# Kernel optimization log

Hardware: AMD Instinct MI355X
Metric: run time of the kernel (lower is better)

Reference implementation:

```python
import jax, jax.numpy as jnp
import numpy as np

B, S, E, H = 4, 2048, 1024, 16
D = E // H  # head_dim = 64

def setup_inputs() -> dict:
    key = jax.random.key(0)
    k1, k2, k3 = jax.random.split(key, 3)
    x = jax.random.normal(k1, (B, S, E), dtype=jnp.float32)
    # nn.Linear(E, 3E, bias=False): y = x @ W^T; we store W already transposed as [E, 3E]
    w_qkv = jax.random.normal(k2, (E, 3 * E), dtype=jnp.float32) * (E ** -0.5)
    w_out = jax.random.normal(k3, (E, E), dtype=jnp.float32) * (E ** -0.5)
    b_out = jnp.zeros((E,), dtype=jnp.float32)
    return {"x": x, "w_qkv": w_qkv, "w_out": w_out, "b_out": b_out}

def reference(x, w_qkv, w_out, b_out):
    b, s, e = x.shape
    h, d = H, e // H
    # qkv projection then rearrange 'b s (qkv h d) -> qkv b h s d'
    qkv = (x @ w_qkv).reshape(b, s, 3, h, d).transpose(2, 0, 3, 1, 4)
    q, k, v = qkv[0], qkv[1], qkv[2]            # each [b, h, s, d]
    scale = jnp.asarray(d, x.dtype) ** -0.5
    att = jnp.einsum('bhxd,bhyd->bhxy', q, k) * scale   # [b, h, s, s]
    att = jax.nn.softmax(att, axis=-1)
    o = jnp.einsum('bhxy,bhyd->bhxd', att, v)           # [b, h, s, d]
    o = o.transpose(0, 2, 1, 3).reshape(b, s, e)        # 'b h s d -> b s (h d)'
    return o @ w_out + b_out
```

## Files before the change

kernel.cpp:

```cpp
#include <hip/hip_runtime.h>
#include <cstdint>
#include <cstddef>


typedef __attribute__((ext_vector_type(8))) short short8;
typedef __attribute__((ext_vector_type(4))) float float4_;
typedef unsigned int u32;
typedef unsigned short u16;

__device__ __forceinline__ u16 f2b(float f) {
  u32 u = __float_as_uint(f);
  u += 0x7FFFu + ((u >> 16) & 1u);
  return (u16)(u >> 16);
}

__device__ __forceinline__ float fexp2(float x) {
#if __has_builtin(__builtin_amdgcn_exp2f)
  return __builtin_amdgcn_exp2f(x);
#else
  return exp2f(x);
#endif
}

__device__ __forceinline__ u32 pk_trunc(float lo, float hi) {
#if __has_builtin(__builtin_amdgcn_perm)
  return __builtin_amdgcn_perm(__float_as_uint(hi), __float_as_uint(lo), 0x07060302);
#else
  return (__float_as_uint(hi) & 0xFFFF0000u) | (__float_as_uint(lo) >> 16);
#endif
}

__device__ __forceinline__ void async_cp16(const void* g, void* l) {
  __builtin_amdgcn_global_load_lds(
      (const __attribute__((address_space(1))) u32*)g,
      (__attribute__((address_space(3))) u32*)l, 16, 0, 0);
}


__global__ void cvt_x_bf16(const float* __restrict__ in, u16* __restrict__ out, int n4) {
  int i = blockIdx.x * 256 + threadIdx.x;
  if (i >= n4) return;
  float4 v = ((const float4*)in)[i];
  uint2 p;
  p.x = (u32)f2b(v.x) | ((u32)f2b(v.y) << 16);
  p.y = (u32)f2b(v.z) | ((u32)f2b(v.w) << 16);
  ((uint2*)out)[i] = p;
}

__global__ void transpose_bf16(const float* __restrict__ in, u16* __restrict__ out,
                               int R, int C) {
  __shared__ float t[32][33];
  int tx = threadIdx.x & 31, ty = threadIdx.x >> 5;
  int r0 = blockIdx.y * 32, c0 = blockIdx.x * 32;
#pragma unroll
  for (int k = 0; k < 4; k++)
    t[ty + 8 * k][tx] = in[(size_t)(r0 + ty + 8 * k) * C + c0 + tx];
  __syncthreads();
#pragma unroll
  for (int k = 0; k < 4; k++)
    out[(size_t)(c0 + ty + 8 * k) * R + r0 + tx] = f2b(t[tx][ty + 8 * k]);
}

__global__ void transpose_v(const u16* __restrict__ V, u16* __restrict__ Vt) {
  __shared__ u16 t[64][80];
  int bh = blockIdx.y, s0 = blockIdx.x * 64;
  const u16* Vh = V + (size_t)bh * 2048 * 64;
  u16* Vth = Vt + (size_t)bh * 64 * 2048;
  int tr = threadIdx.x >> 3;
  int tc = (threadIdx.x & 7) * 8;
#pragma unroll
  for (int p = 0; p < 2; p++) {
    int r = p * 32 + tr;
    *(uint4*)&t[r][tc] = *(const uint4*)(Vh + (size_t)(s0 + r) * 64 + tc);
  }
  __syncthreads();
#pragma unroll
  for (int p = 0; p < 2; p++) {
    int d = p * 32 + tr;
    u16 tmp[8];
#pragma unroll
    for (int k = 0; k < 8; k++) tmp[k] = t[tc + k][d];
    *(uint4*)(Vth + (size_t)d * 2048 + s0 + tc) = *(uint4*)tmp;
  }
}


__global__ __launch_bounds__(256) void gemm_qkv_kernel(
    const u16* __restrict__ A, const u16* __restrict__ Bt,
    u16* __restrict__ QKV) {
  const int K = 1024;
  __shared__ short8 lA[2][512];
  __shared__ short8 lB[2][512];
  int tid = threadIdx.x;
  int w = tid >> 6, l = tid & 63, lr = l & 15, lq = l >> 4;
  int gid = blockIdx.x;
  int xcd = gid & 7, j = gid >> 3;
  int yloc = j & 7, xt = j >> 3;
  int m0 = (xcd * 8 + yloc) * 128, n0 = xt * 128;
  int wm = w & 1, wn = w >> 1;
  float4_ acc[4][4] = {};

  const u16* gA0 = A + (size_t)(m0 + w * 32 + lr) * K + lq * 8;
  const u16* gA1 = gA0 + 16 * K;
  const u16* gB0 = Bt + (size_t)(n0 + w * 32 + lr) * K + lq * 8;
  const u16* gB1 = gB0 + 16 * K;

  auto stage = [&](int buf, int k0) {
    async_cp16(gA0 + k0, &lA[buf][(w * 2 + 0) * 64 + l]);
    async_cp16(gA1 + k0, &lA[buf][(w * 2 + 1) * 64 + l]);
    async_cp16(gB0 + k0, &lB[buf][(w * 2 + 0) * 64 + l]);
    async_cp16(gB1 + k0, &lB[buf][(w * 2 + 1) * 64 + l]);
  };
  auto compute = [&](int buf) {
    short8 af[4], bf[4];
#pragma unroll
    for (int t = 0; t < 4; t++) {
      af[t] = lA[buf][(wm * 4 + t) * 64 + l];
      bf[t] = lB[buf][(wn * 4 + t) * 64 + l];
    }
#pragma unroll
    for (int mt = 0; mt < 4; mt++)
#pragma unroll
      for (int nt = 0; nt < 4; nt++)
        acc[mt][nt] = __builtin_amdgcn_mfma_f32_16x16x32_bf16(af[mt], bf[nt], acc[mt][nt], 0, 0, 0);
  };

  stage(0, 0);
  for (int k0 = 0; k0 < K; k0 += 64) {
    __syncthreads();
    stage(1, k0 + 32);
    compute(0);
    __syncthreads();
    if (k0 + 64 < K) stage(0, k0 + 64);
    compute(1);
  }

  const float qsc = 0.18033688011112042f;
#pragma unroll
  for (int nt = 0; nt < 4; nt++) {
    int gn = n0 + wn * 64 + nt * 16 + lr;
    int sel = gn >> 10;
    int h = (gn >> 6) & 15;
    int d = gn & 63;
    float sc = (sel == 0) ? qsc : 1.0f;
    u16* dst = QKV + (size_t)sel * 8388608 + ((size_t)h * 2048) * 64 + d;
#pragma unroll
    for (int mt = 0; mt < 4; mt++) {
#pragma unroll
      for (int r = 0; r < 4; r++) {
        int gm = m0 + wm * 64 + mt * 16 + lq * 4 + r;
        int b = gm >> 11, s = gm & 2047;
        dst[((size_t)b * 16 * 2048 + s) * 64] = f2b(acc[mt][nt][r] * sc);
      }
    }
  }
}

__global__ __launch_bounds__(256) void gemm_out_kernel(
    const u16* __restrict__ A, const u16* __restrict__ Bt,
    const float* __restrict__ bias, float* __restrict__ out) {
  const int K = 1024;
  __shared__ short8 lA[2][512];
  __shared__ short8 lB[2][512];
  int tid = threadIdx.x;
  int w = tid >> 6, l = tid & 63, lr = l & 15, lq = l >> 4;
  int gid = blockIdx.x;
  int xcd = gid & 7, j = gid >> 3;
  int yloc = j & 7, xt = j >> 3;
  int m0 = (xcd * 8 + yloc) * 128, n0 = xt * 128;
  int wm = w & 1, wn = w >> 1;
  float4_ acc[4][4] = {};

  const u16* gA0 = A + (size_t)(m0 + w * 32 + lr) * K + lq * 8;
  const u16* gA1 = gA0 + 16 * K;
  const u16* gB0 = Bt + (size_t)(n0 + w * 32 + lr) * K + lq * 8;
  const u16* gB1 = gB0 + 16 * K;

  auto stage = [&](int buf, int k0) {
    async_cp16(gA0 + k0, &lA[buf][(w * 2 + 0) * 64 + l]);
    async_cp16(gA1 + k0, &lA[buf][(w * 2 + 1) * 64 + l]);
    async_cp16(gB0 + k0, &lB[buf][(w * 2 + 0) * 64 + l]);
    async_cp16(gB1 + k0, &lB[buf][(w * 2 + 1) * 64 + l]);
  };
  auto compute = [&](int buf) {
    short8 af[4], bf[4];
#pragma unroll
    for (int t = 0; t < 4; t++) {
      af[t] = lA[buf][(wm * 4 + t) * 64 + l];
      bf[t] = lB[buf][(wn * 4 + t) * 64 + l];
    }
#pragma unroll
    for (int mt = 0; mt < 4; mt++)
#pragma unroll
      for (int nt = 0; nt < 4; nt++)
        acc[mt][nt] = __builtin_amdgcn_mfma_f32_16x16x32_bf16(af[mt], bf[nt], acc[mt][nt], 0, 0, 0);
  };

  stage(0, 0);
  for (int k0 = 0; k0 < K; k0 += 64) {
    __syncthreads();
    stage(1, k0 + 32);
    compute(0);
    __syncthreads();
    if (k0 + 64 < K) stage(0, k0 + 64);
    compute(1);
  }

#pragma unroll
  for (int nt = 0; nt < 4; nt++) {
    int gn = n0 + wn * 64 + nt * 16 + lr;
    float bv = bias[gn];
#pragma unroll
    for (int mt = 0; mt < 4; mt++)
#pragma unroll
      for (int r = 0; r < 4; r++) {
        int gm = m0 + wm * 64 + mt * 16 + lq * 4 + r;
        out[(size_t)gm * 1024 + gn] = acc[mt][nt][r] + bv;
      }
  }
}


__global__ __launch_bounds__(256) void attn_kernel(
    const u16* __restrict__ Qb, const u16* __restrict__ Kb,
    const u16* __restrict__ Vt, u16* __restrict__ Ob) {
  const int S = 2048, D = 64;
  __shared__ short8 lK[2][512];
  __shared__ short8 lV[2][512];
  __shared__ __align__(16) u32 pb[4][16][20];
  int tid = threadIdx.x;
  int w = tid >> 6, l = tid & 63, lr = l & 15, lq = l >> 4;
  int gid = blockIdx.x;
  int xcd = gid & 7, j = gid >> 3;
  int bh = xcd * 8 + (j >> 4);
  int qblk = j & 15;
  int q0 = qblk * 128 + w * 32;
  const u16* Qh = Qb + (size_t)bh * S * D;
  const u16* Kh = Kb + (size_t)bh * S * D;
  const u16* Vh = Vt + (size_t)bh * D * S;

  short8 qf[2][2];
#pragma unroll
  for (int qg = 0; qg < 2; qg++) {
    qf[qg][0] = *(const short8*)(Qh + (q0 + qg * 16 + lr) * D + lq * 8);
    qf[qg][1] = *(const short8*)(Qh + (q0 + qg * 16 + lr) * D + 32 + lq * 8);
  }

  float ls[2][4] = {};
  float4_ o[2][4] = {};

  const u16* kg = Kh + (size_t)(((w >> 1) << 5) + 2 * lr + (w & 1)) * D + lq * 8;
  const u16* vg = Vh + (size_t)(w * 16 + lr) * S + lq * 8;

  auto stage = [&](int buf, int kv0) {
    async_cp16(kg + (size_t)kv0 * D, &lK[buf][(w * 2 + 0) * 64 + l]);
    async_cp16(kg + (size_t)kv0 * D + 32, &lK[buf][(w * 2 + 1) * 64 + l]);
    async_cp16(vg + kv0, &lV[buf][(w * 2 + 0) * 64 + l]);
    async_cp16(vg + kv0 + 32, &lV[buf][(w * 2 + 1) * 64 + l]);
  };

  auto compute = [&](int buf) {
#pragma unroll
    for (int sub = 0; sub < 2; sub++) {
      short8 ke0 = lK[buf][((sub * 2 + 0) * 2 + 0) * 64 + l];
      short8 ke1 = lK[buf][((sub * 2 + 0) * 2 + 1) * 64 + l];
      short8 ko0 = lK[buf][((sub * 2 + 1) * 2 + 0) * 64 + l];
      short8 ko1 = lK[buf][((sub * 2 + 1) * 2 + 1) * 64 + l];
#pragma unroll
      for (int qg = 0; qg < 2; qg++) {
        float4_ z = {0.f, 0.f, 0.f, 0.f};
        float4_ s0 = __builtin_amdgcn_mfma_f32_16x16x32_bf16(qf[qg][0], ke0, z, 0, 0, 0);
        s0 = __builtin_amdgcn_mfma_f32_16x16x32_bf16(qf[qg][1], ke1, s0, 0, 0, 0);
        float4_ s1 = __builtin_amdgcn_mfma_f32_16x16x32_bf16(qf[qg][0], ko0, z, 0, 0, 0);
        s1 = __builtin_amdgcn_mfma_f32_16x16x32_bf16(qf[qg][1], ko1, s1, 0, 0, 0);
#pragma unroll
        for (int r = 0; r < 4; r++) {
          float p0 = fexp2(s0[r]);
          float p1 = fexp2(s1[r]);
          u32 pk = pk_trunc(p0, p1);
          ls[qg][r] += __uint_as_float(pk << 16) + __uint_as_float(pk & 0xFFFF0000u);
          pb[w][lq * 4 + r][lr] = pk;
        }
        short8 pa = *(const short8*)&pb[w][lr][lq * 4];
#pragma unroll
        for (int dt = 0; dt < 4; dt++)
          o[qg][dt] = __builtin_amdgcn_mfma_f32_16x16x32_bf16(
              pa, lV[buf][(dt * 2 + sub) * 64 + l], o[qg][dt], 0, 0, 0);
      }
    }
  };

  stage(0, 0);
  for (int kv0 = 0; kv0 < S; kv0 += 128) {
    __syncthreads();
    stage(1, kv0 + 64);
    compute(0);
    __syncthreads();
    if (kv0 + 128 < S) stage(0, kv0 + 128);
    compute(1);
  }

  int b = bh >> 4, h = bh & 15;
#pragma unroll
  for (int qg = 0; qg < 2; qg++) {
    float inv[4];
#pragma unroll
    for (int r = 0; r < 4; r++) {
      float s = ls[qg][r];
#pragma unroll
      for (int off = 1; off < 16; off <<= 1) s += __shfl_xor(s, off, 64);
      inv[r] = 1.0f / s;
    }
#pragma unroll
    for (int dt = 0; dt < 4; dt++)
#pragma unroll
      for (int r = 0; r < 4; r++) {
        int s_ = q0 + qg * 16 + lq * 4 + r;
        Ob[((size_t)(b * 2048 + s_)) * 1024 + h * 64 + dt * 16 + lr] =
            f2b(o[qg][dt][r] * inv[r]);
      }
  }
}


extern "C" void kernel_launch(void* const* d_in, const int* in_sizes, int n_in,
                              void* d_out, int out_size, void* d_ws, size_t ws_size,
                              hipStream_t stream) {
  const float* x     = (const float*)d_in[0];
  const float* w_qkv = (const float*)d_in[1];
  const float* w_out = (const float*)d_in[2];
  const float* b_out = (const float*)d_in[3];
  float* out = (float*)d_out;

  char* ws = (char*)d_ws;
  u16* Xb  = (u16*)(ws);
  u16* Wqt = (u16*)(ws + (16u << 20));
  u16* Wot = (u16*)(ws + (22u << 20));
  u16* QKV = (u16*)(ws + (24u << 20));
  u16* Qb  = QKV;
  u16* Kb  = QKV + 8388608;
  u16* Vb  = QKV + 16777216;
  u16* Vt  = (u16*)(ws + (72u << 20));
  u16* Ob  = Xb;

  cvt_x_bf16<<<8192, 256, 0, stream>>>(x, Xb, 2097152);
  transpose_bf16<<<dim3(96, 32), 256, 0, stream>>>(w_qkv, Wqt, 1024, 3072);
  transpose_bf16<<<dim3(32, 32), 256, 0, stream>>>(w_out, Wot, 1024, 1024);
  gemm_qkv_kernel<<<1536, 256, 0, stream>>>(Xb, Wqt, QKV);
  transpose_v<<<dim3(32, 64), 256, 0, stream>>>(Vb, Vt);
  attn_kernel<<<1024, 256, 0, stream>>>(Qb, Kb, Vt, Ob);
  gemm_out_kernel<<<512, 256, 0, stream>>>(Ob, Wot, b_out, out);
}
```

Before: 350.5 us.

## Fuse prep kernels, use fdot2 for softmax sums, split attention launch

```diff
diff --git a/kernel.cpp b/kernel.cpp
--- a/kernel.cpp
+++ b/kernel.cpp
@@ -30,6 +30,19 @@
 #endif
 }
 
+#if __has_builtin(__builtin_amdgcn_fdot2_f32_bf16)
+typedef __bf16 bf16x2 __attribute__((ext_vector_type(2)));
+__device__ __forceinline__ float accum_pk(u32 pk, float acc) {
+  bf16x2 p = __builtin_bit_cast(bf16x2, pk);
+  bf16x2 one = __builtin_bit_cast(bf16x2, (u32)0x3F803F80u);
+  return __builtin_amdgcn_fdot2_f32_bf16(p, one, acc, false);
+}
+#else
+__device__ __forceinline__ float accum_pk(u32 pk, float acc) {
+  return acc + __uint_as_float(pk << 16) + __uint_as_float(pk & 0xFFFF0000u);
+}
+#endif
+
 __device__ __forceinline__ void async_cp16(const void* g, void* l) {
   __builtin_amdgcn_global_load_lds(
       (const __attribute__((address_space(1))) u32*)g,
@@ -37,21 +50,12 @@
 }
 
 
-__global__ void cvt_x_bf16(const float* __restrict__ in, u16* __restrict__ out, int n4) {
-  int i = blockIdx.x * 256 + threadIdx.x;
-  if (i >= n4) return;
-  float4 v = ((const float4*)in)[i];
-  uint2 p;
-  p.x = (u32)f2b(v.x) | ((u32)f2b(v.y) << 16);
-  p.y = (u32)f2b(v.z) | ((u32)f2b(v.w) << 16);
-  ((uint2*)out)[i] = p;
-}
-
-__global__ void transpose_bf16(const float* __restrict__ in, u16* __restrict__ out,
-                               int R, int C) {
-  __shared__ float t[32][33];
+__device__ __forceinline__ void transpose_block(const float* __restrict__ in,
+                                                u16* __restrict__ out,
+                                                int R, int C, int bx, int by,
+                                                float t[32][33]) {
   int tx = threadIdx.x & 31, ty = threadIdx.x >> 5;
-  int r0 = blockIdx.y * 32, c0 = blockIdx.x * 32;
+  int r0 = by * 32, c0 = bx * 32;
 #pragma unroll
   for (int k = 0; k < 4; k++)
     t[ty + 8 * k][tx] = in[(size_t)(r0 + ty + 8 * k) * C + c0 + tx];
@@ -59,6 +63,27 @@
 #pragma unroll
   for (int k = 0; k < 4; k++)
     out[(size_t)(c0 + ty + 8 * k) * R + r0 + tx] = f2b(t[tx][ty + 8 * k]);
+}
+
+__global__ void prepass_kernel(const float* __restrict__ x, u16* __restrict__ Xb,
+                               const float* __restrict__ wqkv, u16* __restrict__ Wqt,
+                               const float* __restrict__ wout, u16* __restrict__ Wot) {
+  __shared__ float t[32][33];
+  int gid = blockIdx.x;
+  if (gid < 8192) {
+    int i = gid * 256 + threadIdx.x;
+    float4 v = ((const float4*)x)[i];
+    uint2 p;
+    p.x = (u32)f2b(v.x) | ((u32)f2b(v.y) << 16);
+    p.y = (u32)f2b(v.z) | ((u32)f2b(v.w) << 16);
+    ((uint2*)Xb)[i] = p;
+  } else if (gid < 11264) {
+    int j = gid - 8192;
+    transpose_block(wqkv, Wqt, 1024, 3072, j % 96, j / 96, t);
+  } else {
+    int j = gid - 11264;
+    transpose_block(wout, Wot, 1024, 1024, j % 32, j / 32, t);
+  }
 }
 
 __global__ void transpose_v(const u16* __restrict__ V, u16* __restrict__ Vt) {
@@ -223,7 +248,7 @@
 
 __global__ __launch_bounds__(256) void attn_kernel(
     const u16* __restrict__ Qb, const u16* __restrict__ Kb,
-    const u16* __restrict__ Vt, u16* __restrict__ Ob) {
+    const u16* __restrict__ Vt, u16* __restrict__ Ob, int bh_base) {
   const int S = 2048, D = 64;
   __shared__ short8 lK[2][512];
   __shared__ short8 lV[2][512];
@@ -232,7 +257,7 @@
   int w = tid >> 6, l = tid & 63, lr = l & 15, lq = l >> 4;
   int gid = blockIdx.x;
   int xcd = gid & 7, j = gid >> 3;
-  int bh = xcd * 8 + (j >> 4);
+  int bh = bh_base + xcd * 4 + (j >> 4);
   int qblk = j & 15;
   int q0 = qblk * 128 + w * 32;
   const u16* Qh = Qb + (size_t)bh * S * D;
@@ -278,7 +303,7 @@
           float p0 = fexp2(s0[r]);
           float p1 = fexp2(s1[r]);
           u32 pk = pk_trunc(p0, p1);
-          ls[qg][r] += __uint_as_float(pk << 16) + __uint_as_float(pk & 0xFFFF0000u);
+          ls[qg][r] = accum_pk(pk, ls[qg][r]);
           pb[w][lq * 4 + r][lr] = pk;
         }
         short8 pa = *(const short8*)&pb[w][lr][lq * 4];
@@ -343,11 +368,10 @@
   u16* Vt  = (u16*)(ws + (72u << 20));
   u16* Ob  = Xb;
 
-  cvt_x_bf16<<<8192, 256, 0, stream>>>(x, Xb, 2097152);
-  transpose_bf16<<<dim3(96, 32), 256, 0, stream>>>(w_qkv, Wqt, 1024, 3072);
-  transpose_bf16<<<dim3(32, 32), 256, 0, stream>>>(w_out, Wot, 1024, 1024);
+  prepass_kernel<<<12288, 256, 0, stream>>>(x, Xb, w_qkv, Wqt, w_out, Wot);
   gemm_qkv_kernel<<<1536, 256, 0, stream>>>(Xb, Wqt, QKV);
   transpose_v<<<dim3(32, 64), 256, 0, stream>>>(Vb, Vt);
-  attn_kernel<<<1024, 256, 0, stream>>>(Qb, Kb, Vt, Ob);
+  attn_kernel<<<512, 256, 0, stream>>>(Qb, Kb, Vt, Ob, 0);
+  attn_kernel<<<512, 256, 0, stream>>>(Qb, Kb, Vt, Ob, 32);
   gemm_out_kernel<<<512, 256, 0, stream>>>(Ob, Wot, b_out, out);
 }
```

After: 343.3 us. 1.02x faster.
